# Kernel tuning notes

Measured on AMD Instinct MI355X. Metric: run time of the kernel, lower is better.

## Reference

```python
import jax, jax.numpy as jnp
import numpy as np

B, L, H, NH, NE, M = 4, 1024, 768, 12, 42, 8
EMB = 768
OFFSET = 1  # bert cls offset


def setup_inputs() -> dict:
    key = jax.random.key(0)
    ks = jax.random.split(key, 6)
    seq = jax.random.normal(ks[0], (B, L, H), jnp.float32)
    attn = jax.random.uniform(ks[1], (B, NH, L, L), jnp.float32)
    attn = attn / attn.sum(-1, keepdims=True)  # row-stochastic like softmaxed attention probs
    W_head = jax.random.normal(ks[2], (2 * H, EMB), jnp.float32) * 0.02
    b_head = jnp.zeros((EMB,), jnp.float32)
    W_tail = jax.random.normal(ks[3], (2 * H, EMB), jnp.float32) * 0.02
    b_tail = jnp.zeros((EMB,), jnp.float32)
    # mention start positions (before +offset); keep start+offset < L
    mention_pos = jax.random.randint(ks[4], (B, NE, M), 0, L - OFFSET - 1)
    counts = jax.random.randint(ks[5], (B, NE), 1, M + 1)  # >=1 valid mention per entity
    mention_mask = jnp.arange(M)[None, None, :] < counts[:, :, None]
    return dict(sequence_output=seq, attention=attn, W_head=W_head, b_head=b_head,
                W_tail=W_tail, b_tail=b_tail, mention_pos=mention_pos,
                mention_mask=mention_mask)


def _get_hrt(seq, attn, mention_pos, mention_mask):
    # seq: [B,L,H]; attn: [B,NH,L,L]; mention_pos/mask: [B,NE,M]
    b_idx = jnp.arange(B)[:, None, None]
    pos = mention_pos + OFFSET                          # [B,NE,M]
    m_emb = seq[b_idx, pos]                             # [B,NE,M,H] mention embeddings
    att_t = jnp.transpose(attn, (0, 2, 1, 3))           # [B,L,NH,L]
    m_att = att_t[b_idx, pos]                           # [B,NE,M,NH,L] mention attentions
    mask = mention_mask
    neg_inf = jnp.finfo(seq.dtype).min
    # per-entity logsumexp pooling over mentions
    ent_emb = jax.nn.logsumexp(jnp.where(mask[..., None], m_emb, neg_inf), axis=2)
    has_m = mask.any(axis=2)
    ent_emb = jnp.where(has_m[..., None], ent_emb, 0.0)  # [B,NE,H]
    cnt = mask.sum(axis=2).astype(seq.dtype)
    ent_att = (m_att * mask[..., None, None].astype(seq.dtype)).sum(axis=2)
    ent_att = ent_att / jnp.maximum(cnt, 1.0)[..., None, None]  # [B,NE,NH,L] mean over mentions
    # all ordered (head, tail) pairs on the NE x NE grid
    hs = jnp.broadcast_to(ent_emb[:, :, None, :], (B, NE, NE, H))
    ts = jnp.broadcast_to(ent_emb[:, None, :, :], (B, NE, NE, H))
    # ht_att = relu(mean_h(h_att * t_att)), normalized over seq, then context = ht_att @ seq
    ht = jnp.einsum('bihl,bjhl->bijl', ent_att, ent_att) / NH  # [B,NE,NE,L]
    ht = jax.nn.relu(ht)
    ht = ht / (ht.sum(-1, keepdims=True) + 1e-10)
    rs = jnp.einsum('bijl,bld->bijd', ht, seq)                  # [B,NE,NE,H]
    return hs, rs, ts


def reference(sequence_output, attention, W_head, b_head, W_tail, b_tail, mention_pos, mention_mask):
    hs, rs, ts = _get_hrt(sequence_output, attention, mention_pos, mention_mask)
    h_out = jnp.tanh(jnp.concatenate([hs, rs], axis=-1) @ W_head + b_head)
    t_out = jnp.tanh(jnp.concatenate([ts, rs], axis=-1) @ W_tail + b_tail)
    return h_out, t_out
```

## Files before the change

kernel.cpp:

```cpp
#include <hip/hip_runtime.h>
#include <math.h>

typedef _Float16 f16;
typedef __attribute__((ext_vector_type(4))) _Float16 f16x4;
typedef __attribute__((ext_vector_type(8))) _Float16 f16x8;
typedef __attribute__((ext_vector_type(4))) float f32x4;

#define B_    4
#define L_    1024
#define H_    768
#define NH_   12
#define NE_   42
#define M_    8
#define E2_   1536
#define HTP_  1792
#define OUT_HALF 5419008LL

__global__ void k_ent_emb(const float* __restrict__ seq,
                          const int* __restrict__ mpos,
                          const int* __restrict__ mmask,
                          f16* __restrict__ ent) {
    int e = blockIdx.x, b = blockIdx.y;
    int tid = threadIdx.x;
    const int* mp = mpos  + (b*NE_ + e)*M_;
    const int* mk = mmask + (b*NE_ + e)*M_;
    int pos[M_], msk[M_];
#pragma unroll
    for (int m = 0; m < M_; m++) { msk[m] = mk[m]; pos[m] = mp[m] + 1; }
#pragma unroll
    for (int q = 0; q < 3; q++) {
        int h = tid + q*256;
        float mx = -1e30f, vals[M_];
#pragma unroll
        for (int m = 0; m < M_; m++) {
            vals[m] = 0.f;
            if (msk[m]) {
                float v = seq[((long long)b*L_ + pos[m])*H_ + h];
                vals[m] = v; mx = fmaxf(mx, v);
            }
        }
        float s = 0.f;
#pragma unroll
        for (int m = 0; m < M_; m++) if (msk[m]) s += expf(vals[m] - mx);
        float lse = (mx > -1e29f) ? mx + logf(s) : 0.f;
        ent[(b*NE_ + e)*H_ + h] = (f16)lse;
    }
}

__global__ void k_ent_att(const float* __restrict__ attn,
                          const int* __restrict__ mpos,
                          const int* __restrict__ mmask,
                          float* __restrict__ eatt) {
    int nh = blockIdx.x, e = blockIdx.y, b = blockIdx.z;
    int tid = threadIdx.x;
    int l0 = tid * 4;
    const int* mp = mpos  + (b*NE_ + e)*M_;
    const int* mk = mmask + (b*NE_ + e)*M_;
    const float* abase = attn + (long long)(b*NH_ + nh) * L_ * L_;
    f32x4 acc = {0,0,0,0}; int cnt = 0;
#pragma unroll
    for (int m = 0; m < M_; m++) {
        if (mk[m]) {
            cnt++;
            const float* row = abase + (long long)(mp[m] + 1) * L_;
            acc += *(const f32x4*)(row + l0);
        }
    }
    float inv = 1.f / (float)(cnt > 0 ? cnt : 1);
    acc *= inv;
    *(f32x4*)(eatt + ((long long)(b*NE_ + e)*NH_ + nh)*L_ + l0) = acc;
}

__global__ void k_ht(const float* __restrict__ eatt, f16* __restrict__ HT) {
    int j = blockIdx.x, i = blockIdx.y, b = blockIdx.z;
    int tid = threadIdx.x;
    int l0 = tid * 4;
    const float* ei = eatt + (long long)(b*NE_ + i)*NH_*L_;
    const float* ej = eatt + (long long)(b*NE_ + j)*NH_*L_;
    f32x4 acc = {0,0,0,0};
#pragma unroll
    for (int h = 0; h < NH_; h++) {
        f32x4 vi = *(const f32x4*)(ei + h*L_ + l0);
        f32x4 vj = *(const f32x4*)(ej + h*L_ + l0);
        acc += vi * vj;
    }
    float v[4]; float s = 0.f;
#pragma unroll
    for (int r = 0; r < 4; r++) {
        float t = acc[r] * (1.f/12.f);
        t = t > 0.f ? t : 0.f;
        v[r] = t; s += t;
    }
    int wave = tid >> 6, lane = tid & 63;
#pragma unroll
    for (int m = 1; m < 64; m <<= 1) s += __shfl_xor(s, m, 64);
    __shared__ float red[4];
    if (lane == 0) red[wave] = s;
    __syncthreads();
    float S = red[0] + red[1] + red[2] + red[3];
    float sc = 1.f / (S + 1e-10f);
    f16x4 o = {(f16)(v[0]*sc), (f16)(v[1]*sc), (f16)(v[2]*sc), (f16)(v[3]*sc)};
    *(f16x4*)(HT + ((long long)b*HTP_ + i*NE_ + j)*L_ + l0) = o;
}

__global__ void k_prep(const float* __restrict__ Wh, const float* __restrict__ bh,
                       const float* __restrict__ Wt, const float* __restrict__ bt,
                       f16* __restrict__ wtop, f16* __restrict__ wbot,
                       float* __restrict__ bcat) {
    int idx = blockIdx.x*256 + threadIdx.x;
    if (idx < E2_*H_) {
        int c = idx / H_;
        int h = idx - c*H_;
        float tp, bo;
        if (c < H_) { tp = Wh[h*H_ + c];          bo = Wh[(H_ + h)*H_ + c]; }
        else        { tp = Wt[h*H_ + (c - H_)];   bo = Wt[(H_ + h)*H_ + (c - H_)]; }
        wtop[idx] = (f16)tp; wbot[idx] = (f16)bo;
    }
    if (idx < E2_) bcat[idx] = (idx < H_) ? bh[idx] : bt[idx - H_];
}

__global__ void k_seq16(const float* __restrict__ seq, f16* __restrict__ seq16) {
    int idx = (blockIdx.x*256 + threadIdx.x) * 4;
    f32x4 v = *(const f32x4*)(seq + idx);
    f16x4 o = {(f16)v[0], (f16)v[1], (f16)v[2], (f16)v[3]};
    *(f16x4*)(seq16 + idx) = o;
}

#define BM 64
#define BN 64
#define BK 32
#define LDSS 40

template<int MODE>
__global__ __launch_bounds__(256)
void k_gemm(const f16* __restrict__ A, const f16* __restrict__ BT,
            int M, int K, long long strideA, long long strideBT,
            float* __restrict__ het, const float* __restrict__ bcat,
            float* __restrict__ outp, f16* __restrict__ outp16) {
    __shared__ __align__(16) f16 As[BM*LDSS];
    __shared__ __align__(16) f16 Bs[BN*LDSS];
    int bm = blockIdx.x*BM, bn = blockIdx.y*BN, bz = blockIdx.z;
    const f16* Ab = A + strideA*bz;
    const f16* Bb = BT + strideBT*bz;
    int tid = threadIdx.x;
    int wave = tid >> 6, lane = tid & 63;
    int wm = (wave >> 1)*32, wn = (wave & 1)*32;
    int lo4 = lane & 15, kq = (lane >> 4)*8;
    int srow = tid >> 2, scol = (tid & 3)*8;
    bool aval = (bm + srow) < M;
    const f16* aptr = Ab + (long long)(bm + srow)*K + scol;
    const f16* bptr = Bb + (long long)(bn + srow)*K + scol;
    f32x4 acc[2][2] = {};
    for (int k0 = 0; k0 < K; k0 += BK) {
        uint4 zero = {0,0,0,0};
        uint4 av = aval ? *(const uint4*)(aptr + k0) : zero;
        uint4 bv = *(const uint4*)(bptr + k0);
        __syncthreads();
        *(uint4*)(As + srow*LDSS + scol) = av;
        *(uint4*)(Bs + srow*LDSS + scol) = bv;
        __syncthreads();
        f16x8 a0 = *(const f16x8*)(As + (wm +      lo4)*LDSS + kq);
        f16x8 a1 = *(const f16x8*)(As + (wm + 16 + lo4)*LDSS + kq);
        f16x8 b0 = *(const f16x8*)(Bs + (wn +      lo4)*LDSS + kq);
        f16x8 b1 = *(const f16x8*)(Bs + (wn + 16 + lo4)*LDSS + kq);
        acc[0][0] = __builtin_amdgcn_mfma_f32_16x16x32_f16(a0, b0, acc[0][0], 0,0,0);
        acc[0][1] = __builtin_amdgcn_mfma_f32_16x16x32_f16(a0, b1, acc[0][1], 0,0,0);
        acc[1][0] = __builtin_amdgcn_mfma_f32_16x16x32_f16(a1, b0, acc[1][0], 0,0,0);
        acc[1][1] = __builtin_amdgcn_mfma_f32_16x16x32_f16(a1, b1, acc[1][1], 0,0,0);
    }
    int rloc = (lane >> 4)*4;
#pragma unroll
    for (int sm = 0; sm < 2; sm++)
#pragma unroll
    for (int sn = 0; sn < 2; sn++) {
        f32x4 a = acc[sm][sn];
        int c  = bn + wn + sn*16 + lo4;
        int rb = bm + wm + sm*16 + rloc;
        if constexpr (MODE == 0) {
#pragma unroll
            for (int r = 0; r < 4; r++)
                if (rb + r < M) het[(rb + r)*E2_ + c] = a[r] + bcat[c];
        } else if constexpr (MODE == 1) {
            f16x4 o = {(f16)a[0], (f16)a[1], (f16)a[2], (f16)a[3]};
            *(f16x4*)(outp16 + (long long)bz*E2_*L_ + (long long)c*L_ + rb) = o;
        } else {
#pragma unroll
            for (int r = 0; r < 4; r++) {
                int row = rb + r;
                if (row < M) {
                    int i = row / NE_;
                    int j = row - i*NE_;
                    int sel = (c < H_) ? i : j;
                    float bias = het[(bz*NE_ + sel)*E2_ + c];
                    float v = tanhf(a[r] + bias);
                    long long o = (c < H_)
                        ? ((long long)((bz*NE_ + i)*NE_ + j))*H_ + c
                        : OUT_HALF + ((long long)((bz*NE_ + i)*NE_ + j))*H_ + (c - H_);
                    outp[o] = v;
                }
            }
        }
    }
}

extern "C" void kernel_launch(void* const* d_in, const int* in_sizes, int n_in,
                              void* d_out, int out_size, void* d_ws, size_t ws_size,
                              hipStream_t stream) {
    const float* seq  = (const float*)d_in[0];
    const float* attn = (const float*)d_in[1];
    const float* Wh   = (const float*)d_in[2];
    const float* bh   = (const float*)d_in[3];
    const float* Wt   = (const float*)d_in[4];
    const float* bt   = (const float*)d_in[5];
    const int* mpos   = (const int*)d_in[6];
    const int* mmask  = (const int*)d_in[7];
    float* out = (float*)d_out;
    char* ws = (char*)d_ws;
    f16*   ent   = (f16*)  (ws + 0);
    f16*   wtop  = (f16*)  (ws + 258048);
    f16*   wbot  = (f16*)  (ws + 2617344);
    float* bcat  = (float*)(ws + 4976640);
    float* het   = (float*)(ws + 4982784);
    float* eatt  = (float*)(ws + 6014976);
    f16*   HT    = (f16*)  (ws + 14272512);
    f16*   seqWT = (f16*)  (ws + 28952576);
    f16*   seq16 = (f16*)  (ws + 6014976);

    k_prep   <<<4608, 256, 0, stream>>>(Wh, bh, Wt, bt, wtop, wbot, bcat);
    k_ent_emb<<<dim3(NE_, B_), 256, 0, stream>>>(seq, mpos, mmask, ent);
    k_ent_att<<<dim3(NH_, NE_, B_), 256, 0, stream>>>(attn, mpos, mmask, eatt);
    k_ht     <<<dim3(NE_, NE_, B_), 256, 0, stream>>>(eatt, HT);
    k_seq16  <<<3072, 256, 0, stream>>>(seq, seq16);
    k_gemm<0><<<dim3(3, 24, 1), 256, 0, stream>>>(ent, wtop, 168, 768, 0, 0,
        het, bcat, nullptr, nullptr);
    k_gemm<1><<<dim3(16, 24, B_), 256, 0, stream>>>(seq16, wbot, 1024, 768,
        (long long)L_*H_, 0, nullptr, nullptr, nullptr, seqWT);
    k_gemm<2><<<dim3(28, 24, B_), 256, 0, stream>>>(HT, seqWT, 1764, 1024,
        (long long)HTP_*L_, (long long)E2_*L_, het, nullptr, out, nullptr);
}
```

Baseline: 429.7 us.

## Retile GEMMs to 128x128 with async LDS loads and restructure prep kernels

Replaces the 64x64 GEMMs for the seq@W and HT@seqWT stages with 128x128 tiles that use global_load_lds direct-to-LDS copies and a 4x4 MFMA grid per wave. It also stores entity attention in fp16 and caches the i-row in LDS so each k_ht block handles 7 j-pairs. The weight transpose in k_prep now goes through a shared-memory tile so both reads and writes are coalesced. These changes target GEMM tile-load overhead, redundant eatt traffic and uncoalesced transpose writes. The costs are an unswizzled LDS layout that may cause bank conflicts, a single LDS buffer with no prefetch, and extra fp16 rounding of the attention averages.

```diff
diff --git a/kernel.cpp b/kernel.cpp
--- a/kernel.cpp
+++ b/kernel.cpp
@@ -16,6 +16,12 @@
 #define HTP_  1792
 #define OUT_HALF 5419008LL
 
+typedef __attribute__((address_space(1))) const unsigned char ga_t;
+typedef __attribute__((address_space(3))) unsigned char la_t;
+__device__ __forceinline__ void async16(const void* g, void* l) {
+    __builtin_amdgcn_global_load_lds((ga_t*)g, (la_t*)l, 16, 0, 0);
+}
+
 __global__ void k_ent_emb(const float* __restrict__ seq,
                           const int* __restrict__ mpos,
                           const int* __restrict__ mmask,
@@ -50,7 +56,7 @@
 __global__ void k_ent_att(const float* __restrict__ attn,
                           const int* __restrict__ mpos,
                           const int* __restrict__ mmask,
-                          float* __restrict__ eatt) {
+                          f16* __restrict__ eatt) {
     int nh = blockIdx.x, e = blockIdx.y, b = blockIdx.z;
     int tid = threadIdx.x;
     int l0 = tid * 4;
@@ -67,56 +73,82 @@
         }
     }
     float inv = 1.f / (float)(cnt > 0 ? cnt : 1);
-    acc *= inv;
-    *(f32x4*)(eatt + ((long long)(b*NE_ + e)*NH_ + nh)*L_ + l0) = acc;
-}
-
-__global__ void k_ht(const float* __restrict__ eatt, f16* __restrict__ HT) {
-    int j = blockIdx.x, i = blockIdx.y, b = blockIdx.z;
+    f16x4 o = {(f16)(acc[0]*inv), (f16)(acc[1]*inv), (f16)(acc[2]*inv), (f16)(acc[3]*inv)};
+    *(f16x4*)(eatt + ((long long)(b*NE_ + e)*NH_ + nh)*L_ + l0) = o;
+}
+
+__global__ __launch_bounds__(256) void k_ht(const f16* __restrict__ eatt,
+                                            f16* __restrict__ HT) {
+    int jg = blockIdx.x, i = blockIdx.y, b = blockIdx.z;
     int tid = threadIdx.x;
-    int l0 = tid * 4;
-    const float* ei = eatt + (long long)(b*NE_ + i)*NH_*L_;
-    const float* ej = eatt + (long long)(b*NE_ + j)*NH_*L_;
-    f32x4 acc = {0,0,0,0};
-#pragma unroll
-    for (int h = 0; h < NH_; h++) {
-        f32x4 vi = *(const f32x4*)(ei + h*L_ + l0);
-        f32x4 vj = *(const f32x4*)(ej + h*L_ + l0);
-        acc += vi * vj;
-    }
-    float v[4]; float s = 0.f;
+    __shared__ __align__(16) f16 ei_s[NH_*L_];
+    __shared__ float red[4];
+    const f16* ei = eatt + (long long)(b*NE_ + i)*NH_*L_;
+#pragma unroll
+    for (int q = 0; q < 6; q++) {
+        int off = (q*256 + tid)*8;
+        *(f16x8*)(ei_s + off) = *(const f16x8*)(ei + off);
+    }
+    __syncthreads();
+    int l0 = tid*4;
+    int wave = tid >> 6, lane = tid & 63;
+    for (int jj = 0; jj < 7; jj++) {
+        int j = jg*7 + jj;
+        const f16* ej = eatt + (long long)(b*NE_ + j)*NH_*L_;
+        f32x4 acc = {0,0,0,0};
+#pragma unroll
+        for (int h = 0; h < NH_; h++) {
+            f16x4 vi = *(const f16x4*)(ei_s + h*L_ + l0);
+            f16x4 vj = *(const f16x4*)(ej   + h*L_ + l0);
+#pragma unroll
+            for (int r = 0; r < 4; r++) acc[r] += (float)vi[r] * (float)vj[r];
+        }
+        float v[4]; float s = 0.f;
+#pragma unroll
+        for (int r = 0; r < 4; r++) {
+            float t = acc[r] * (1.f/12.f);
+            t = t > 0.f ? t : 0.f;
+            v[r] = t; s += t;
+        }
+#pragma unroll
+        for (int m = 1; m < 64; m <<= 1) s += __shfl_xor(s, m, 64);
+        if (lane == 0) red[wave] = s;
+        __syncthreads();
+        float S = red[0] + red[1] + red[2] + red[3];
+        __syncthreads();
+        float sc = 1.f / (S + 1e-10f);
+        f16x4 o = {(f16)(v[0]*sc), (f16)(v[1]*sc), (f16)(v[2]*sc), (f16)(v[3]*sc)};
+        *(f16x4*)(HT + ((long long)b*HTP_ + i*NE_ + j)*L_ + l0) = o;
+    }
+}
+
+__global__ __launch_bounds__(256)
+void k_prep(const float* __restrict__ Wh, const float* __restrict__ Wt,
+            const float* __restrict__ bh, const float* __restrict__ bt,
+            f16* __restrict__ wtop, f16* __restrict__ wbot,
+            float* __restrict__ bcat) {
+    __shared__ float tile[32][33];
+    int tx = blockIdx.x, ty = blockIdx.y, m = blockIdx.z;
+    const float* src = (m & 1) ? Wt : Wh;
+    int roff = (m & 2) ? H_ : 0;
+    f16* dst = (m & 2) ? wbot : wtop;
+    int coff = (m & 1) ? H_ : 0;
+    int x = threadIdx.x & 31, y8 = threadIdx.x >> 5;
 #pragma unroll
     for (int r = 0; r < 4; r++) {
-        float t = acc[r] * (1.f/12.f);
-        t = t > 0.f ? t : 0.f;
-        v[r] = t; s += t;
-    }
-    int wave = tid >> 6, lane = tid & 63;
-#pragma unroll
-    for (int m = 1; m < 64; m <<= 1) s += __shfl_xor(s, m, 64);
-    __shared__ float red[4];
-    if (lane == 0) red[wave] = s;
+        int h = ty*32 + y8 + r*8, c = tx*32 + x;
+        tile[y8 + r*8][x] = src[(long long)(roff + h)*H_ + c];
+    }
     __syncthreads();
-    float S = red[0] + red[1] + red[2] + red[3];
-    float sc = 1.f / (S + 1e-10f);
-    f16x4 o = {(f16)(v[0]*sc), (f16)(v[1]*sc), (f16)(v[2]*sc), (f16)(v[3]*sc)};
-    *(f16x4*)(HT + ((long long)b*HTP_ + i*NE_ + j)*L_ + l0) = o;
-}
-
-__global__ void k_prep(const float* __restrict__ Wh, const float* __restrict__ bh,
-                       const float* __restrict__ Wt, const float* __restrict__ bt,
-                       f16* __restrict__ wtop, f16* __restrict__ wbot,
-                       float* __restrict__ bcat) {
-    int idx = blockIdx.x*256 + threadIdx.x;
-    if (idx < E2_*H_) {
-        int c = idx / H_;
-        int h = idx - c*H_;
-        float tp, bo;
-        if (c < H_) { tp = Wh[h*H_ + c];          bo = Wh[(H_ + h)*H_ + c]; }
-        else        { tp = Wt[h*H_ + (c - H_)];   bo = Wt[(H_ + h)*H_ + (c - H_)]; }
-        wtop[idx] = (f16)tp; wbot[idx] = (f16)bo;
-    }
-    if (idx < E2_) bcat[idx] = (idx < H_) ? bh[idx] : bt[idx - H_];
+#pragma unroll
+    for (int r = 0; r < 4; r++) {
+        int c2 = tx*32 + y8 + r*8, h2 = ty*32 + x;
+        dst[(long long)(coff + c2)*H_ + h2] = (f16)tile[x][y8 + r*8];
+    }
+    if (tx == 0 && ty == 0 && m == 0) {
+        for (int idx = threadIdx.x; idx < E2_; idx += 256)
+            bcat[idx] = (idx < H_) ? bh[idx] : bt[idx - H_];
+    }
 }
 
 __global__ void k_seq16(const float* __restrict__ seq, f16* __restrict__ seq16) {
@@ -126,32 +158,23 @@
     *(f16x4*)(seq16 + idx) = o;
 }
 
-#define BM 64
-#define BN 64
-#define BK 32
 #define LDSS 40
-
-template<int MODE>
 __global__ __launch_bounds__(256)
-void k_gemm(const f16* __restrict__ A, const f16* __restrict__ BT,
-            int M, int K, long long strideA, long long strideBT,
-            float* __restrict__ het, const float* __restrict__ bcat,
-            float* __restrict__ outp, f16* __restrict__ outp16) {
-    __shared__ __align__(16) f16 As[BM*LDSS];
-    __shared__ __align__(16) f16 Bs[BN*LDSS];
-    int bm = blockIdx.x*BM, bn = blockIdx.y*BN, bz = blockIdx.z;
-    const f16* Ab = A + strideA*bz;
-    const f16* Bb = BT + strideBT*bz;
+void k_gemm_het(const f16* __restrict__ A, const f16* __restrict__ BT,
+                int M, int K, float* __restrict__ het, const float* __restrict__ bcat) {
+    __shared__ __align__(16) f16 As[64*LDSS];
+    __shared__ __align__(16) f16 Bs[64*LDSS];
+    int bm = blockIdx.x*64, bn = blockIdx.y*64;
     int tid = threadIdx.x;
     int wave = tid >> 6, lane = tid & 63;
     int wm = (wave >> 1)*32, wn = (wave & 1)*32;
     int lo4 = lane & 15, kq = (lane >> 4)*8;
     int srow = tid >> 2, scol = (tid & 3)*8;
     bool aval = (bm + srow) < M;
-    const f16* aptr = Ab + (long long)(bm + srow)*K + scol;
-    const f16* bptr = Bb + (long long)(bn + srow)*K + scol;
+    const f16* aptr = A + (long long)(bm + srow)*K + scol;
+    const f16* bptr = BT + (long long)(bn + srow)*K + scol;
     f32x4 acc[2][2] = {};
-    for (int k0 = 0; k0 < K; k0 += BK) {
+    for (int k0 = 0; k0 < K; k0 += 32) {
         uint4 zero = {0,0,0,0};
         uint4 av = aval ? *(const uint4*)(aptr + k0) : zero;
         uint4 bv = *(const uint4*)(bptr + k0);
@@ -176,18 +199,67 @@
         f32x4 a = acc[sm][sn];
         int c  = bn + wn + sn*16 + lo4;
         int rb = bm + wm + sm*16 + rloc;
-        if constexpr (MODE == 0) {
-#pragma unroll
-            for (int r = 0; r < 4; r++)
-                if (rb + r < M) het[(rb + r)*E2_ + c] = a[r] + bcat[c];
-        } else if constexpr (MODE == 1) {
+#pragma unroll
+        for (int r = 0; r < 4; r++)
+            if (rb + r < M) het[(rb + r)*E2_ + c] = a[r] + bcat[c];
+    }
+}
+
+template<int MODE>
+__global__ __launch_bounds__(256)
+void k_gemm2(const f16* __restrict__ A, const f16* __restrict__ BT, int K,
+             long long strideA, long long strideBT,
+             const float* __restrict__ het, float* __restrict__ outp,
+             f16* __restrict__ outp16) {
+    __shared__ __align__(16) f16 As[128*32];
+    __shared__ __align__(16) f16 Bs[128*32];
+    int bm = blockIdx.x*128, bn = blockIdx.y*128, bz = blockIdx.z;
+    const f16* Ab = A + strideA*bz;
+    const f16* Bb = BT + strideBT*bz;
+    int tid = threadIdx.x, wave = tid >> 6, lane = tid & 63;
+    int wm = (wave >> 1)*64, wn = (wave & 1)*64;
+    int lo4 = lane & 15, kq = (lane >> 4)*8;
+    int lrow = lane >> 2, lcol = (lane & 3)*8;
+    const f16* ag = Ab + (long long)(bm + wave*32 + lrow)*K + lcol;
+    const f16* bg = Bb + (long long)(bn + wave*32 + lrow)*K + lcol;
+    f16* asl = As + wave*1024;
+    f16* bsl = Bs + wave*1024;
+    f32x4 acc[4][4] = {};
+    for (int k0 = 0; k0 < K; k0 += 32) {
+        async16(ag + k0,          asl);
+        async16(ag + k0 + 16*K,   asl + 512);
+        async16(bg + k0,          bsl);
+        async16(bg + k0 + 16*K,   bsl + 512);
+        __syncthreads();
+        f16x8 af[4], bf[4];
+#pragma unroll
+        for (int s = 0; s < 4; s++) {
+            af[s] = *(const f16x8*)(As + (wm + s*16 + lo4)*32 + kq);
+            bf[s] = *(const f16x8*)(Bs + (wn + s*16 + lo4)*32 + kq);
+        }
+#pragma unroll
+        for (int sm = 0; sm < 4; sm++)
+#pragma unroll
+        for (int sn = 0; sn < 4; sn++)
+            acc[sm][sn] = __builtin_amdgcn_mfma_f32_16x16x32_f16(af[sm], bf[sn], acc[sm][sn], 0,0,0);
+        __syncthreads();
+    }
+    int rloc = (lane >> 4)*4;
+#pragma unroll
+    for (int sm = 0; sm < 4; sm++)
+#pragma unroll
+    for (int sn = 0; sn < 4; sn++) {
+        f32x4 a = acc[sm][sn];
+        int c  = bn + wn + sn*16 + lo4;
+        int rb = bm + wm + sm*16 + rloc;
+        if constexpr (MODE == 1) {
             f16x4 o = {(f16)a[0], (f16)a[1], (f16)a[2], (f16)a[3]};
             *(f16x4*)(outp16 + (long long)bz*E2_*L_ + (long long)c*L_ + rb) = o;
         } else {
 #pragma unroll
             for (int r = 0; r < 4; r++) {
                 int row = rb + r;
-                if (row < M) {
+                if (row < NE_*NE_) {
                     int i = row / NE_;
                     int j = row - i*NE_;
                     int sel = (c < H_) ? i : j;
@@ -221,20 +293,19 @@
     f16*   wbot  = (f16*)  (ws + 2617344);
     float* bcat  = (float*)(ws + 4976640);
     float* het   = (float*)(ws + 4982784);
-    float* eatt  = (float*)(ws + 6014976);
-    f16*   HT    = (f16*)  (ws + 14272512);
-    f16*   seqWT = (f16*)  (ws + 28952576);
-    f16*   seq16 = (f16*)  (ws + 6014976);
-
-    k_prep   <<<4608, 256, 0, stream>>>(Wh, bh, Wt, bt, wtop, wbot, bcat);
+    f16*   eatt  = (f16*)  (ws + 6014976);
+    f16*   seq16 = (f16*)  (ws + 10143744);
+    f16*   HT    = (f16*)  (ws + 16435200);
+    f16*   seqWT = (f16*)  (ws + 31115264);
+
+    k_prep   <<<dim3(24, 24, 4), 256, 0, stream>>>(Wh, Wt, bh, bt, wtop, wbot, bcat);
     k_ent_emb<<<dim3(NE_, B_), 256, 0, stream>>>(seq, mpos, mmask, ent);
     k_ent_att<<<dim3(NH_, NE_, B_), 256, 0, stream>>>(attn, mpos, mmask, eatt);
-    k_ht     <<<dim3(NE_, NE_, B_), 256, 0, stream>>>(eatt, HT);
+    k_ht     <<<dim3(6, NE_, B_), 256, 0, stream>>>(eatt, HT);
     k_seq16  <<<3072, 256, 0, stream>>>(seq, seq16);
-    k_gemm<0><<<dim3(3, 24, 1), 256, 0, stream>>>(ent, wtop, 168, 768, 0, 0,
-        het, bcat, nullptr, nullptr);
-    k_gemm<1><<<dim3(16, 24, B_), 256, 0, stream>>>(seq16, wbot, 1024, 768,
-        (long long)L_*H_, 0, nullptr, nullptr, nullptr, seqWT);
-    k_gemm<2><<<dim3(28, 24, B_), 256, 0, stream>>>(HT, seqWT, 1764, 1024,
-        (long long)HTP_*L_, (long long)E2_*L_, het, nullptr, out, nullptr);
-}
+    k_gemm_het<<<dim3(3, 24, 1), 256, 0, stream>>>(ent, wtop, 168, 768, het, bcat);
+    k_gemm2<1><<<dim3(8, 12, B_), 256, 0, stream>>>(seq16, wbot, 768,
+        (long long)L_*H_, 0, nullptr, nullptr, seqWT);
+    k_gemm2<2><<<dim3(14, 12, B_), 256, 0, stream>>>(HT, seqWT, 1024,
+        (long long)HTP_*L_, (long long)E2_*L_, het, out, nullptr);
+}
```

Measured after the change: 403.6 us. 6.1% less time.
